# Optimization experiments

Hardware: AMD Instinct MI355X
Metric: run time of the kernel (lower is better)

The kernel has to match this reference:

```python
import jax, jax.numpy as jnp
import numpy as np
from jax import lax

C = 384
B, H, W = 16, 56, 56
EPS = 1e-5
KS = [5, 7, 7, 3, 3, 3]
DIL = [1, 1, 2, 3, 4, 5]


def _dwconv(x, w, dilation):
    # depthwise conv, groups == channels; SAME-style padding (r*(k-1)+1)//2
    k = w.shape[-1]
    p = (dilation * (k - 1) + 1) // 2
    return lax.conv_general_dilated(
        x, w, window_strides=(1, 1), padding=[(p, p), (p, p)],
        rhs_dilation=(dilation, dilation),
        dimension_numbers=('NCHW', 'OIHW', 'NCHW'),
        feature_group_count=x.shape[1])


def _bn(x, p):
    # inference-mode BatchNorm2d: p = [gamma, beta, running_mean, running_var], each [C]
    g, b, m, v = p[0], p[1], p[2], p[3]
    scale = (g * lax.rsqrt(v + EPS)).reshape(1, -1, 1, 1)
    shift = (b - m * g * lax.rsqrt(v + EPS)).reshape(1, -1, 1, 1)
    return x * scale + shift


def setup_inputs() -> dict:
    key = jax.random.key(0)
    ks = jax.random.split(key, 10)
    inp = {
        'x': jax.random.normal(ks[0], (B, C, H, W), jnp.float32),
        'lk_w': jax.random.normal(ks[1], (C, 1, 13, 13), jnp.float32) * 0.05,
        'obn': jax.random.uniform(ks[2], (4, C), jnp.float32),
        'w5': jax.random.normal(ks[3], (C, 1, 5, 5), jnp.float32) * 0.05,
        'w7a': jax.random.normal(ks[4], (C, 1, 7, 7), jnp.float32) * 0.05,
        'w7b': jax.random.normal(ks[5], (C, 1, 7, 7), jnp.float32) * 0.05,
        'w3a': jax.random.normal(ks[6], (C, 1, 3, 3), jnp.float32) * 0.05,
        'w3b': jax.random.normal(ks[7], (C, 1, 3, 3), jnp.float32) * 0.05,
        'w3c': jax.random.normal(ks[8], (C, 1, 3, 3), jnp.float32) * 0.05,
        'br_bn': jax.random.uniform(ks[9], (6, 4, C), jnp.float32),
    }
    return inp


def reference(x, lk_w, obn, w5, w7a, w7b, w3a, w3b, w3c, br_bn):
    out = _bn(_dwconv(x, lk_w, 1), obn)  # origin 13x13 branch
    ws = [w5, w7a, w7b, w3a, w3b, w3c]
    for i, (w, r) in enumerate(zip(ws, DIL)):
        out = out + _bn(_dwconv(x, w, r), br_bn[i])
    return out
```

## Files before the change

### kernel.cpp

```cpp
#include <hip/hip_runtime.h>
#include <hip/hip_bf16.h>

#define C_ 384
#define B_ 16
#define H_ 56
#define W_ 56
#define WROW_ 8
#define SPSZ_ 4944

typedef _Float16 f16x8 __attribute__((ext_vector_type(8)));
typedef float    f32x4 __attribute__((ext_vector_type(4)));

__device__ __forceinline__ float foldw(int c, int py, int px,
    const float* lk, const float* w5, const float* w7a, const float* w7b,
    const float* w3a, const float* w3b, const float* w3c, const float* sc)
{
    int dy = py - 6, dx = px - 6;
    float a = sc[0] * lk[c * 169 + py * 13 + px];
#define ADDBR(Wp, K, R, SI)                                               \
    {                                                                     \
        const int half = ((K) - 1) / 2;                                   \
        if (dy % (R) == 0 && dx % (R) == 0) {                             \
            int iy = dy / (R), ix = dx / (R);                             \
            if (iy >= -half && iy <= half && ix >= -half && ix <= half)   \
                a += sc[SI] * Wp[c * (K) * (K) + (iy + half) * (K) + (ix + half)]; \
        }                                                                 \
    }
    ADDBR(w5,  5, 1, 1)
    ADDBR(w7a, 7, 1, 2)
    ADDBR(w7b, 7, 2, 3)
    ADDBR(w3a, 3, 3, 4)
    ADDBR(w3b, 3, 4, 5)
    ADDBR(w3c, 3, 5, 6)
#undef ADDBR
    return a;
}

__global__ void build_weights_kernel(
    const float* __restrict__ lk, const float* __restrict__ obn,
    const float* __restrict__ w5, const float* __restrict__ w7a,
    const float* __restrict__ w7b, const float* __restrict__ w3a,
    const float* __restrict__ w3b, const float* __restrict__ w3c,
    const float* __restrict__ brbn,
    unsigned* __restrict__ wpk, float* __restrict__ bias)
{
    int c = blockIdx.x;
    int t = threadIdx.x;

    float sc[7], sh[7];
    {
        float g = obn[c], b = obn[C_ + c], m = obn[2 * C_ + c], v = obn[3 * C_ + c];
        float s = g * rsqrtf(v + 1e-5f);
        sc[0] = s; sh[0] = b - m * s;
    }
#pragma unroll
    for (int i = 0; i < 6; ++i) {
        float g = brbn[(i * 4 + 0) * C_ + c], b = brbn[(i * 4 + 1) * C_ + c];
        float m = brbn[(i * 4 + 2) * C_ + c], v = brbn[(i * 4 + 3) * C_ + c];
        float s = g * rsqrtf(v + 1e-5f);
        sc[i + 1] = s; sh[i + 1] = b - m * s;
    }

    if (t < 13 * WROW_) {
        int ky = t / WROW_, pp = t % WROW_;
        int kx0 = 2 * pp, kx1 = 2 * pp + 1;
        float w0 = (kx0 < 13) ? foldw(c, ky, kx0, lk, w5, w7a, w7b, w3a, w3b, w3c, sc) : 0.f;
        float w1 = (kx1 < 13) ? foldw(c, ky, kx1, lk, w5, w7a, w7b, w3a, w3b, w3c, sc) : 0.f;
        _Float16 h0 = (_Float16)w0, h1 = (_Float16)w1;
        unsigned u = ((unsigned)__builtin_bit_cast(unsigned short, h1) << 16)
                   |  (unsigned)__builtin_bit_cast(unsigned short, h0);
        wpk[c * 13 * WROW_ + t] = u;
    }
    if (t == 0) {
        float s = 0.f;
#pragma unroll
        for (int i = 0; i < 7; ++i) s += sh[i];
        bias[c] = s;
    }
}

__global__ __launch_bounds__(256, 5) void dwconv13_mfma(
    const float* __restrict__ x, const unsigned* __restrict__ wpk,
    const float* __restrict__ bias, float* __restrict__ out)
{
    __shared__ unsigned sP[SPSZ_];
    __shared__ unsigned sQ[320];

    const int bid = blockIdx.x;
    const int c   = bid % C_;
    const int bg  = bid / C_;
    const int b0  = bg * 2;
    const int t   = threadIdx.x;

    unsigned vv[13]; int dd[13];
#pragma unroll
    for (int k = 0; k < 13; ++k) {
        int slot = t + k * 256;
        if (k < 12 || slot < 3136) {
            int p  = slot / 1568, rem = slot - p * 1568;
            int iy = rem / 28,    pr  = rem - iy * 28;
            const float* xp = x + ((size_t)((b0 + p) * C_ + c)) * (H_ * W_);
            float2 v = *(const float2*)(xp + iy * W_ + pr * 2);
            _Float16 h0 = (_Float16)v.x, h1 = (_Float16)v.y;
            vv[k] = ((unsigned)__builtin_bit_cast(unsigned short, h1) << 16)
                  |  (unsigned)__builtin_bit_cast(unsigned short, h0);
            dd[k] = p * 2448 + (iy + 6) * 36 + 3 + pr;
        }
    }
#pragma unroll
    for (int k = 0; k < 2; ++k) {
        int s = t + k * 256;
        if (s < 320) {
            unsigned q = 0;
            if (s < 312) {
                int ky = s / 24, t24 = s - ky * 24;
                if (t24 >= 8 && t24 < 16) q = wpk[c * 104 + ky * 8 + (t24 - 8)];
            }
            sQ[s] = q;
        }
    }
    {
        uint4 z = make_uint4(0u, 0u, 0u, 0u);
        uint4* s4 = (uint4*)sP;
#pragma unroll
        for (int k = 0; k < 5; ++k) {
            int slot = t + k * 256;
            if (k < 4 || slot < SPSZ_ / 4) s4[slot] = z;
        }
    }
    __syncthreads();

#pragma unroll
    for (int k = 0; k < 13; ++k) {
        int slot = t + k * 256;
        if (k < 12 || slot < 3136) sP[dd[k]] = vv[k];
    }
    __syncthreads();

    const float bv  = bias[c];
    const int lane = t & 63;
    const int wv   = t >> 6;
    const int x0   = wv * 16;
    const int g    = lane >> 4, n = lane & 15;
    const int r8   = lane & 7,  pp = (lane >> 3) & 1;

    const int q0 = 16 + 8 * g - n;
    const int v0 = q0 >> 1;
    const unsigned shb = (unsigned)(q0 & 1) * 16u;
    f16x8 bf[13];
#pragma unroll
    for (int ky = 0; ky < 13; ++ky) {
        const unsigned* Q = sQ + ky * 24 + v0;
        unsigned U0 = Q[0], U1 = Q[1], U2 = Q[2], U3 = Q[3], U4 = Q[4];
        uint4 u;
        u.x = __builtin_amdgcn_alignbit(U1, U0, shb);
        u.y = __builtin_amdgcn_alignbit(U2, U1, shb);
        u.z = __builtin_amdgcn_alignbit(U3, U2, shb);
        u.w = __builtin_amdgcn_alignbit(U4, U3, shb);
        bf[ky] = __builtin_bit_cast(f16x8, u);
    }

    const int aBase = pp * 2448 + r8 * 36 + x0 / 2 + 4 * g;
    const int xo = x0 + n;

#pragma unroll
    for (int ty = 0; ty < 7; ++ty) {
        f32x4 d0 = { bv, bv, bv, bv };
        f32x4 d1 = { 0.f, 0.f, 0.f, 0.f };
        int base = aBase + (8 * ty) * 36;
        uint4 ua = *(const uint4*)(sP + base);
#pragma unroll
        for (int ky = 0; ky < 13; ++ky) {
            uint4 un;
            if (ky < 12) un = *(const uint4*)(sP + base + (ky + 1) * 36);
            f16x8 a = __builtin_bit_cast(f16x8, ua);
            if (ky & 1) d1 = __builtin_amdgcn_mfma_f32_16x16x32_f16(a, bf[ky], d1, 0, 0, 0);
            else        d0 = __builtin_amdgcn_mfma_f32_16x16x32_f16(a, bf[ky], d0, 0, 0, 0);
            if (ky < 12) ua = un;
        }
        d0 = d0 + d1;
        if (xo < W_) {
#pragma unroll
            for (int r = 0; r < 4; ++r) {
                int m  = 4 * g + r;
                int p2 = m >> 3, rr = m & 7;
                out[((size_t)((b0 + p2) * C_ + c)) * (H_ * W_)
                    + (8 * ty + rr) * W_ + xo] = d0[r];
            }
        }
    }
}

extern "C" void kernel_launch(void* const* d_in, const int* in_sizes, int n_in,
                              void* d_out, int out_size, void* d_ws, size_t ws_size,
                              hipStream_t stream) {
    const float* x    = (const float*)d_in[0];
    const float* lk   = (const float*)d_in[1];
    const float* obn  = (const float*)d_in[2];
    const float* w5   = (const float*)d_in[3];
    const float* w7a  = (const float*)d_in[4];
    const float* w7b  = (const float*)d_in[5];
    const float* w3a  = (const float*)d_in[6];
    const float* w3b  = (const float*)d_in[7];
    const float* w3c  = (const float*)d_in[8];
    const float* brbn = (const float*)d_in[9];
    float* out  = (float*)d_out;

    unsigned* wpk  = (unsigned*)d_ws;
    float*    bias = (float*)(wpk + C_ * 13 * WROW_);

    hipLaunchKernelGGL(build_weights_kernel, dim3(C_), dim3(128), 0, stream,
                       lk, obn, w5, w7a, w7b, w3a, w3b, w3c, brbn, wpk, bias);

    hipLaunchKernelGGL(dwconv13_mfma, dim3((B_ / 2) * C_), dim3(256), 0, stream,
                       x, wpk, bias, out);
}
```

Baseline: 41.71 us.

## Prebuild padded weight rows in global, drop LDS weight stage, reuse row registers

The weight builder now writes the padded 24-wide weight rows straight to global memory. The conv kernel then reads B fragments directly from global instead of staging them in LDS, which removes the sQ buffer and its loads. The inner loop now keeps the 5 overlapping input rows in registers across output tiles, so each tile reads only 8 new LDS rows instead of 13. Launch bounds drop from 5 to 4 waves per SIMD to make room for the extra registers, at the cost of occupancy.

```diff
diff --git a/kernel.cpp b/kernel.cpp
--- a/kernel.cpp
+++ b/kernel.cpp
@@ -5,8 +5,9 @@
 #define B_ 16
 #define H_ 56
 #define W_ 56
-#define WROW_ 8
 #define SPSZ_ 4944
+#define WQROW_ 24
+#define WQSZ_ 320
 
 typedef _Float16 f16x8 __attribute__((ext_vector_type(8)));
 typedef float    f32x4 __attribute__((ext_vector_type(4)));
@@ -42,7 +43,7 @@
     const float* __restrict__ w7b, const float* __restrict__ w3a,
     const float* __restrict__ w3b, const float* __restrict__ w3c,
     const float* __restrict__ brbn,
-    unsigned* __restrict__ wpk, float* __restrict__ bias)
+    unsigned* __restrict__ wq, float* __restrict__ bias)
 {
     int c = blockIdx.x;
     int t = threadIdx.x;
@@ -61,15 +62,22 @@
         sc[i + 1] = s; sh[i + 1] = b - m * s;
     }
 
-    if (t < 13 * WROW_) {
-        int ky = t / WROW_, pp = t % WROW_;
-        int kx0 = 2 * pp, kx1 = 2 * pp + 1;
-        float w0 = (kx0 < 13) ? foldw(c, ky, kx0, lk, w5, w7a, w7b, w3a, w3b, w3c, sc) : 0.f;
-        float w1 = (kx1 < 13) ? foldw(c, ky, kx1, lk, w5, w7a, w7b, w3a, w3b, w3c, sc) : 0.f;
-        _Float16 h0 = (_Float16)w0, h1 = (_Float16)w1;
-        unsigned u = ((unsigned)__builtin_bit_cast(unsigned short, h1) << 16)
-                   |  (unsigned)__builtin_bit_cast(unsigned short, h0);
-        wpk[c * 13 * WROW_ + t] = u;
+#pragma unroll
+    for (int k = 0; k < 3; ++k) {
+        int s = t + k * 128;
+        if (s < WQSZ_) {
+            unsigned u = 0;
+            int ky = s / WQROW_, t24 = s - ky * WQROW_;
+            if (ky < 13 && t24 >= 8 && t24 < 16) {
+                int kx0 = 2 * (t24 - 8), kx1 = kx0 + 1;
+                float w0 = (kx0 < 13) ? foldw(c, ky, kx0, lk, w5, w7a, w7b, w3a, w3b, w3c, sc) : 0.f;
+                float w1 = (kx1 < 13) ? foldw(c, ky, kx1, lk, w5, w7a, w7b, w3a, w3b, w3c, sc) : 0.f;
+                _Float16 h0 = (_Float16)w0, h1 = (_Float16)w1;
+                u = ((unsigned)__builtin_bit_cast(unsigned short, h1) << 16)
+                  |  (unsigned)__builtin_bit_cast(unsigned short, h0);
+            }
+            wq[c * WQSZ_ + s] = u;
+        }
     }
     if (t == 0) {
         float s = 0.f;
@@ -79,12 +87,11 @@
     }
 }
 
-__global__ __launch_bounds__(256, 5) void dwconv13_mfma(
-    const float* __restrict__ x, const unsigned* __restrict__ wpk,
+__global__ __launch_bounds__(256, 4) void dwconv13_mfma(
+    const float* __restrict__ x, const unsigned* __restrict__ wq,
     const float* __restrict__ bias, float* __restrict__ out)
 {
     __shared__ unsigned sP[SPSZ_];
-    __shared__ unsigned sQ[320];
 
     const int bid = blockIdx.x;
     const int c   = bid % C_;
@@ -107,50 +114,17 @@
             dd[k] = p * 2448 + (iy + 6) * 36 + 3 + pr;
         }
     }
-#pragma unroll
-    for (int k = 0; k < 2; ++k) {
-        int s = t + k * 256;
-        if (s < 320) {
-            unsigned q = 0;
-            if (s < 312) {
-                int ky = s / 24, t24 = s - ky * 24;
-                if (t24 >= 8 && t24 < 16) q = wpk[c * 104 + ky * 8 + (t24 - 8)];
-            }
-            sQ[s] = q;
-        }
-    }
-    {
-        uint4 z = make_uint4(0u, 0u, 0u, 0u);
-        uint4* s4 = (uint4*)sP;
-#pragma unroll
-        for (int k = 0; k < 5; ++k) {
-            int slot = t + k * 256;
-            if (k < 4 || slot < SPSZ_ / 4) s4[slot] = z;
-        }
-    }
-    __syncthreads();
-
-#pragma unroll
-    for (int k = 0; k < 13; ++k) {
-        int slot = t + k * 256;
-        if (k < 12 || slot < 3136) sP[dd[k]] = vv[k];
-    }
-    __syncthreads();
-
-    const float bv  = bias[c];
+
     const int lane = t & 63;
-    const int wv   = t >> 6;
-    const int x0   = wv * 16;
     const int g    = lane >> 4, n = lane & 15;
-    const int r8   = lane & 7,  pp = (lane >> 3) & 1;
-
     const int q0 = 16 + 8 * g - n;
     const int v0 = q0 >> 1;
     const unsigned shb = (unsigned)(q0 & 1) * 16u;
+    const unsigned* Wq = wq + c * WQSZ_ + v0;
     f16x8 bf[13];
 #pragma unroll
     for (int ky = 0; ky < 13; ++ky) {
-        const unsigned* Q = sQ + ky * 24 + v0;
+        const unsigned* Q = Wq + ky * WQROW_;
         unsigned U0 = Q[0], U1 = Q[1], U2 = Q[2], U3 = Q[3], U4 = Q[4];
         uint4 u;
         u.x = __builtin_amdgcn_alignbit(U1, U0, shb);
@@ -160,25 +134,57 @@
         bf[ky] = __builtin_bit_cast(f16x8, u);
     }
 
+    {
+        uint4 z = make_uint4(0u, 0u, 0u, 0u);
+        uint4* s4 = (uint4*)sP;
+#pragma unroll
+        for (int k = 0; k < 5; ++k) {
+            int slot = t + k * 256;
+            if (k < 4 || slot < SPSZ_ / 4) s4[slot] = z;
+        }
+    }
+    __syncthreads();
+
+#pragma unroll
+    for (int k = 0; k < 13; ++k) {
+        int slot = t + k * 256;
+        if (k < 12 || slot < 3136) sP[dd[k]] = vv[k];
+    }
+    __syncthreads();
+
+    const float bv  = bias[c];
+    const int wv   = t >> 6;
+    const int x0   = wv * 16;
+    const int r8   = lane & 7,  pp = (lane >> 3) & 1;
+
     const int aBase = pp * 2448 + r8 * 36 + x0 / 2 + 4 * g;
     const int xo = x0 + n;
 
+#define RDF(R) (*(const uint4*)(sP + aBase + (R) * 36))
+
+    uint4 S[5];
+#pragma unroll
+    for (int j = 0; j < 5; ++j) S[j] = RDF(j);
+
 #pragma unroll
     for (int ty = 0; ty < 7; ++ty) {
+        uint4 T[8];
+#pragma unroll
+        for (int j = 0; j < 8; ++j) T[j] = RDF(8 * ty + 5 + j);
+
         f32x4 d0 = { bv, bv, bv, bv };
         f32x4 d1 = { 0.f, 0.f, 0.f, 0.f };
-        int base = aBase + (8 * ty) * 36;
-        uint4 ua = *(const uint4*)(sP + base);
 #pragma unroll
         for (int ky = 0; ky < 13; ++ky) {
-            uint4 un;
-            if (ky < 12) un = *(const uint4*)(sP + base + (ky + 1) * 36);
-            f16x8 a = __builtin_bit_cast(f16x8, ua);
+            f16x8 a = __builtin_bit_cast(f16x8, (ky < 5) ? S[ky] : T[ky - 5]);
             if (ky & 1) d1 = __builtin_amdgcn_mfma_f32_16x16x32_f16(a, bf[ky], d1, 0, 0, 0);
             else        d0 = __builtin_amdgcn_mfma_f32_16x16x32_f16(a, bf[ky], d0, 0, 0, 0);
-            if (ky < 12) ua = un;
         }
         d0 = d0 + d1;
+
+#pragma unroll
+        for (int j = 0; j < 5; ++j) S[j] = T[3 + j];
+
         if (xo < W_) {
 #pragma unroll
             for (int r = 0; r < 4; ++r) {
@@ -189,6 +195,7 @@
             }
         }
     }
+#undef RDF
 }
 
 extern "C" void kernel_launch(void* const* d_in, const int* in_sizes, int n_in,
@@ -206,12 +213,12 @@
     const float* brbn = (const float*)d_in[9];
     float* out  = (float*)d_out;
 
-    unsigned* wpk  = (unsigned*)d_ws;
-    float*    bias = (float*)(wpk + C_ * 13 * WROW_);
+    unsigned* wq   = (unsigned*)d_ws;
+    float*    bias = (float*)(wq + C_ * WQSZ_);
 
     hipLaunchKernelGGL(build_weights_kernel, dim3(C_), dim3(128), 0, stream,
-                       lk, obn, w5, w7a, w7b, w3a, w3b, w3c, brbn, wpk, bias);
+                       lk, obn, w5, w7a, w7b, w3a, w3b, w3c, brbn, wq, bias);
 
     hipLaunchKernelGGL(dwconv13_mfma, dim3((B_ / 2) * C_), dim3(256), 0, stream,
-                       x, wpk, bias, out);
-}
+                       x, wq, bias, out);
+}
```

New measurement: 57.94 us. +38.9%, slower.

## Reuse each LDS A-fragment across all output row tiles with seven accumulators

Applied to the files above, without the earlier changes.

Restructures the MFMA loop so each padded input row fragment is read from LDS once and fed to every output row tile that uses it, keeping seven accumulator vectors live. Before, each of the seven row tiles reloaded its thirteen overlapping rows. Row loads are double-buffered in groups of four. The extra live registers force the launch-bounds occupancy hint down from 5 to 3, which may reduce latency hiding.

```diff
diff --git a/kernel.cpp b/kernel.cpp
--- a/kernel.cpp
+++ b/kernel.cpp
@@ -79,7 +79,7 @@
     }
 }
 
-__global__ __launch_bounds__(256, 5) void dwconv13_mfma(
+__global__ __launch_bounds__(256, 3) void dwconv13_mfma(
     const float* __restrict__ x, const unsigned* __restrict__ wpk,
     const float* __restrict__ bias, float* __restrict__ out)
 {
@@ -163,29 +163,56 @@
     const int aBase = pp * 2448 + r8 * 36 + x0 / 2 + 4 * g;
     const int xo = x0 + n;
 
-#pragma unroll
-    for (int ty = 0; ty < 7; ++ty) {
-        f32x4 d0 = { bv, bv, bv, bv };
-        f32x4 d1 = { 0.f, 0.f, 0.f, 0.f };
-        int base = aBase + (8 * ty) * 36;
-        uint4 ua = *(const uint4*)(sP + base);
-#pragma unroll
-        for (int ky = 0; ky < 13; ++ky) {
-            uint4 un;
-            if (ky < 12) un = *(const uint4*)(sP + base + (ky + 1) * 36);
-            f16x8 a = __builtin_bit_cast(f16x8, ua);
-            if (ky & 1) d1 = __builtin_amdgcn_mfma_f32_16x16x32_f16(a, bf[ky], d1, 0, 0, 0);
-            else        d0 = __builtin_amdgcn_mfma_f32_16x16x32_f16(a, bf[ky], d0, 0, 0, 0);
-            if (ky < 12) ua = un;
-        }
-        d0 = d0 + d1;
-        if (xo < W_) {
+#define RDF(R) (*(const uint4*)(sP + aBase + (R) * 36))
+
+    f32x4 d[7];
+#pragma unroll
+    for (int ty = 0; ty < 7; ++ty) d[ty] = (f32x4){ bv, bv, bv, bv };
+
+    uint4 FA[4], FB[4];
+#pragma unroll
+    for (int i = 0; i < 4; ++i) FA[i] = RDF(i);
+
+#pragma unroll
+    for (int Gp = 0; Gp < 16; ++Gp) {
+        if (Gp < 15) {
+#pragma unroll
+            for (int i = 0; i < 4; ++i) {
+                int r = 4 * (Gp + 1) + i;
+                if (r <= 60) {
+                    if (Gp & 1) FA[i] = RDF(r);
+                    else        FB[i] = RDF(r);
+                }
+            }
+        }
+#pragma unroll
+        for (int i = 0; i < 4; ++i) {
+            int r = 4 * Gp + i;
+            if (r <= 60) {
+                uint4 fv = (Gp & 1) ? FB[i] : FA[i];
+                f16x8 a = __builtin_bit_cast(f16x8, fv);
+                int tyHi = r >> 3; if (tyHi > 6) tyHi = 6;
+                int tyLo = (r >= 13) ? ((r - 5) >> 3) : 0;
+#pragma unroll
+                for (int ty = 0; ty < 7; ++ty) {
+                    if (ty >= tyLo && ty <= tyHi)
+                        d[ty] = __builtin_amdgcn_mfma_f32_16x16x32_f16(
+                                    a, bf[r - 8 * ty], d[ty], 0, 0, 0);
+                }
+            }
+        }
+    }
+#undef RDF
+
+    if (xo < W_) {
+#pragma unroll
+        for (int ty = 0; ty < 7; ++ty) {
 #pragma unroll
             for (int r = 0; r < 4; ++r) {
                 int m  = 4 * g + r;
                 int p2 = m >> 3, rr = m & 7;
                 out[((size_t)((b0 + p2) * C_ + c)) * (H_ * W_)
-                    + (8 * ty + rr) * W_ + xo] = d0[r];
+                    + (8 * ty + rr) * W_ + xo] = d[ty][r];
             }
         }
     }
```

After: 42.35 us. About the same (+1.6%).

## Process two batch pairs per block with double-buffered LDS and prefetch

Applied to the files above, without the earlier changes.

Each block now handles four images (two pairs) of one channel instead of two, with a second LDS buffer. Global loads for the second pair are issued before the MFMA compute on the first pair, so load latency overlaps compute, and the weight/sQ setup is amortised over twice the work. In exchange the grid is halved, LDS per block roughly doubles, and the occupancy hint drops from 5 to 3 blocks, which may reduce latency hiding across blocks.

```diff
diff --git a/kernel.cpp b/kernel.cpp
--- a/kernel.cpp
+++ b/kernel.cpp
@@ -79,53 +79,69 @@
     }
 }
 
-__global__ __launch_bounds__(256, 5) void dwconv13_mfma(
+__global__ __launch_bounds__(256, 3) void dwconv13_mfma(
     const float* __restrict__ x, const unsigned* __restrict__ wpk,
     const float* __restrict__ bias, float* __restrict__ out)
 {
-    __shared__ unsigned sP[SPSZ_];
+    __shared__ unsigned sPd[2][SPSZ_];
     __shared__ unsigned sQ[320];
 
     const int bid = blockIdx.x;
     const int c   = bid % C_;
-    const int bg  = bid / C_;
-    const int b0  = bg * 2;
+    const int q   = bid / C_;
     const int t   = threadIdx.x;
 
-    unsigned vv[13]; int dd[13];
+    int dd[13];
+    unsigned vv[13];
+
+#define STAGE_ISSUE(b0v)                                                    \
+    {                                                                       \
+        _Pragma("unroll")                                                   \
+        for (int k = 0; k < 13; ++k) {                                      \
+            int slot = t + k * 256;                                         \
+            if (k < 12 || slot < 3136) {                                    \
+                int p  = slot / 1568, rem = slot - p * 1568;                \
+                int iy = rem / 28,    pr  = rem - iy * 28;                  \
+                const float* xp = x + ((size_t)(((b0v) + p) * C_ + c)) * (H_ * W_); \
+                float2 v = *(const float2*)(xp + iy * W_ + pr * 2);         \
+                _Float16 h0 = (_Float16)v.x, h1 = (_Float16)v.y;            \
+                vv[k] = ((unsigned)__builtin_bit_cast(unsigned short, h1) << 16) \
+                      |  (unsigned)__builtin_bit_cast(unsigned short, h0);  \
+            }                                                               \
+        }                                                                   \
+    }
+
 #pragma unroll
     for (int k = 0; k < 13; ++k) {
         int slot = t + k * 256;
         if (k < 12 || slot < 3136) {
             int p  = slot / 1568, rem = slot - p * 1568;
             int iy = rem / 28,    pr  = rem - iy * 28;
-            const float* xp = x + ((size_t)((b0 + p) * C_ + c)) * (H_ * W_);
-            float2 v = *(const float2*)(xp + iy * W_ + pr * 2);
-            _Float16 h0 = (_Float16)v.x, h1 = (_Float16)v.y;
-            vv[k] = ((unsigned)__builtin_bit_cast(unsigned short, h1) << 16)
-                  |  (unsigned)__builtin_bit_cast(unsigned short, h0);
             dd[k] = p * 2448 + (iy + 6) * 36 + 3 + pr;
-        }
-    }
+        } else dd[k] = 0;
+    }
+
+    STAGE_ISSUE(4 * q)
 #pragma unroll
     for (int k = 0; k < 2; ++k) {
         int s = t + k * 256;
         if (s < 320) {
-            unsigned q = 0;
+            unsigned qv = 0;
             if (s < 312) {
                 int ky = s / 24, t24 = s - ky * 24;
-                if (t24 >= 8 && t24 < 16) q = wpk[c * 104 + ky * 8 + (t24 - 8)];
+                if (t24 >= 8 && t24 < 16) qv = wpk[c * 104 + ky * 8 + (t24 - 8)];
             }
-            sQ[s] = q;
+            sQ[s] = qv;
         }
     }
     {
         uint4 z = make_uint4(0u, 0u, 0u, 0u);
-        uint4* s4 = (uint4*)sP;
-#pragma unroll
-        for (int k = 0; k < 5; ++k) {
+        uint4* s4 = (uint4*)&sPd[0][0];
+        const int tot4 = (2 * SPSZ_) / 4;
+#pragma unroll
+        for (int k = 0; k < 10; ++k) {
             int slot = t + k * 256;
-            if (k < 4 || slot < SPSZ_ / 4) s4[slot] = z;
+            if (k < 9 || slot < tot4) s4[slot] = z;
         }
     }
     __syncthreads();
@@ -133,7 +149,7 @@
 #pragma unroll
     for (int k = 0; k < 13; ++k) {
         int slot = t + k * 256;
-        if (k < 12 || slot < 3136) sP[dd[k]] = vv[k];
+        if (k < 12 || slot < 3136) sPd[0][dd[k]] = vv[k];
     }
     __syncthreads();
 
@@ -163,32 +179,52 @@
     const int aBase = pp * 2448 + r8 * 36 + x0 / 2 + 4 * g;
     const int xo = x0 + n;
 
-#pragma unroll
-    for (int ty = 0; ty < 7; ++ty) {
-        f32x4 d0 = { bv, bv, bv, bv };
-        f32x4 d1 = { 0.f, 0.f, 0.f, 0.f };
-        int base = aBase + (8 * ty) * 36;
-        uint4 ua = *(const uint4*)(sP + base);
-#pragma unroll
-        for (int ky = 0; ky < 13; ++ky) {
-            uint4 un;
-            if (ky < 12) un = *(const uint4*)(sP + base + (ky + 1) * 36);
-            f16x8 a = __builtin_bit_cast(f16x8, ua);
-            if (ky & 1) d1 = __builtin_amdgcn_mfma_f32_16x16x32_f16(a, bf[ky], d1, 0, 0, 0);
-            else        d0 = __builtin_amdgcn_mfma_f32_16x16x32_f16(a, bf[ky], d0, 0, 0, 0);
-            if (ky < 12) ua = un;
-        }
-        d0 = d0 + d1;
-        if (xo < W_) {
-#pragma unroll
-            for (int r = 0; r < 4; ++r) {
-                int m  = 4 * g + r;
-                int p2 = m >> 3, rr = m & 7;
-                out[((size_t)((b0 + p2) * C_ + c)) * (H_ * W_)
-                    + (8 * ty + rr) * W_ + xo] = d0[r];
-            }
-        }
-    }
+#define COMPUTE(BUF, b0v)                                                   \
+    {                                                                       \
+        const unsigned* sp = &sPd[BUF][0];                                  \
+        _Pragma("unroll")                                                   \
+        for (int ty = 0; ty < 7; ++ty) {                                    \
+            f32x4 d0 = { bv, bv, bv, bv };                                  \
+            f32x4 d1 = { 0.f, 0.f, 0.f, 0.f };                              \
+            int base = aBase + (8 * ty) * 36;                               \
+            uint4 ua = *(const uint4*)(sp + base);                          \
+            _Pragma("unroll")                                               \
+            for (int ky = 0; ky < 13; ++ky) {                               \
+                uint4 un;                                                   \
+                if (ky < 12) un = *(const uint4*)(sp + base + (ky + 1) * 36); \
+                f16x8 a = __builtin_bit_cast(f16x8, ua);                    \
+                if (ky & 1) d1 = __builtin_amdgcn_mfma_f32_16x16x32_f16(a, bf[ky], d1, 0, 0, 0); \
+                else        d0 = __builtin_amdgcn_mfma_f32_16x16x32_f16(a, bf[ky], d0, 0, 0, 0); \
+                if (ky < 12) ua = un;                                       \
+            }                                                               \
+            d0 = d0 + d1;                                                   \
+            if (xo < W_) {                                                  \
+                _Pragma("unroll")                                           \
+                for (int r = 0; r < 4; ++r) {                               \
+                    int m  = 4 * g + r;                                     \
+                    int p2 = m >> 3, rr = m & 7;                            \
+                    out[((size_t)(((b0v) + p2) * C_ + c)) * (H_ * W_)       \
+                        + (8 * ty + rr) * W_ + xo] = d0[r];                 \
+                }                                                           \
+            }                                                               \
+        }                                                                   \
+    }
+
+    STAGE_ISSUE(4 * q + 2)
+
+    COMPUTE(0, 4 * q)
+
+#pragma unroll
+    for (int k = 0; k < 13; ++k) {
+        int slot = t + k * 256;
+        if (k < 12 || slot < 3136) sPd[1][dd[k]] = vv[k];
+    }
+    __syncthreads();
+
+    COMPUTE(1, 4 * q + 2)
+
+#undef COMPUTE
+#undef STAGE_ISSUE
 }
 
 extern "C" void kernel_launch(void* const* d_in, const int* in_sizes, int n_in,
@@ -212,6 +248,6 @@
     hipLaunchKernelGGL(build_weights_kernel, dim3(C_), dim3(128), 0, stream,
                        lk, obn, w5, w7a, w7b, w3a, w3b, w3c, brbn, wpk, bias);
 
-    hipLaunchKernelGGL(dwconv13_mfma, dim3((B_ / 2) * C_), dim3(256), 0, stream,
+    hipLaunchKernelGGL(dwconv13_mfma, dim3((B_ / 4) * C_), dim3(256), 0, stream,
                        x, wpk, bias, out);
 }
```

Result: slower. 43.61 us (+4.6%).
